# Performance work log

Measured on AMD Instinct MI355X. Metric: run time of the kernel, lower is better.

The kernel has to match this reference:

```python
import jax, jax.numpy as jnp
import numpy as np

MC, IN_C, OUT_C, K, STRIDE, PAD = 10, 16, 32, 3, 2, 1
D = IN_C * K * K  # 144


def setup_inputs() -> dict:
    key = jax.random.key(0)
    k1, k2 = jax.random.split(key)
    x = jax.random.normal(k1, (8, IN_C, 128, 128), dtype=jnp.float32)
    theta_logsigma = jnp.zeros((1,), jnp.float32)
    Omega_mean = jnp.zeros((D, OUT_C), jnp.float32)
    # init: theta_llscale * -2 = -log(in*k*k)
    Omega_logsigma = jnp.full((D, OUT_C), -np.log(float(D)), jnp.float32)
    Omega_eps = jax.random.normal(k2, (MC, D, OUT_C), dtype=jnp.float32)
    return {"x": x, "theta_logsigma": theta_logsigma, "Omega_mean": Omega_mean,
            "Omega_logsigma": Omega_logsigma, "Omega_eps": Omega_eps}


def reference(x, theta_logsigma, Omega_mean, Omega_logsigma, Omega_eps):
    B, _, H, W = x.shape
    # reparameterized weights: [mc, D, out]
    Omega = Omega_eps * jnp.exp(Omega_logsigma * 0.5) + Omega_mean
    # torch: view(mc,k,k,in,out).permute(0,4,3,1,2).reshape(mc*out,in,k,k)
    w = Omega.reshape(MC, K, K, IN_C, OUT_C).transpose(0, 4, 3, 1, 2)
    w = w.reshape(MC * OUT_C, IN_C, K, K)
    # F0 path: replicate x over mc -> [B, mc*in, H, W]
    xr = jnp.broadcast_to(x[None], (MC, B, IN_C, H, W)).transpose(1, 0, 2, 3, 4)
    xr = xr.reshape(B, MC * IN_C, H, W)
    phi_half = jax.lax.conv_general_dilated(
        xr, w, window_strides=(STRIDE, STRIDE),
        padding=[(PAD, PAD), (PAD, PAD)],
        dimension_numbers=("NCHW", "OIHW", "NCHW"),
        feature_group_count=MC)
    hw = phi_half.shape[-1]
    N_rf = OUT_C * hw * hw
    scale = jnp.exp(0.5 * theta_logsigma[0]) / jnp.sqrt(jnp.asarray(N_rf, x.dtype))
    ph = phi_half.reshape(B, MC, OUT_C, hw, hw)
    phi = jnp.concatenate([scale * jnp.cos(ph), scale * jnp.sin(ph)], axis=2)
    return phi.reshape(B, MC * 2 * OUT_C, hw, hw)
```

## Files before the change

kernel.cpp:

```cpp
#include <hip/hip_runtime.h>
#include <hip/hip_bf16.h>
#include <math.h>

#define MC_    10
#define IN_C_  16
#define OUT_C_ 32
#define K_     3
#define D_     (IN_C_ * K_ * K_)
#define H_     128
#define W_     128
#define HW_    64
#define B_     8

__global__ __launch_bounds__(256) void prep_w_kernel(
    const float* __restrict__ eps, const float* __restrict__ logsig,
    const float* __restrict__ mean, float* __restrict__ w)
{
    int i = blockIdx.x * 256 + threadIdx.x;
    if (i < MC_ * D_ * OUT_C_) {
        int doc = i % (D_ * OUT_C_);
        w[i] = eps[i] * __expf(0.5f * logsig[doc]) + mean[doc];
    }
}

__global__ __launch_bounds__(256) void conv_rff_kernel(
    const float* __restrict__ x,
    const float* __restrict__ w,
    const float* __restrict__ theta,
    float* __restrict__ out)
{
    const int tid    = threadIdx.x;
    const int lane   = tid & 63;
    const int waveid = tid >> 6;
    const int oh     = blockIdx.x * 4 + waveid;
    const int mc     = blockIdx.y;
    const int b      = blockIdx.z;
    const int ow     = lane;

    const float scale = __expf(0.5f * theta[0]) *
                        rsqrtf((float)(OUT_C_ * HW_ * HW_));

    float acc[OUT_C_];
#pragma unroll
    for (int oc = 0; oc < OUT_C_; ++oc) acc[oc] = 0.0f;

    const float* __restrict__ wmc = w + (size_t)mc * (D_ * OUT_C_);
    const float* __restrict__ xb  = x + (size_t)b * IN_C_ * H_ * W_;
    const int ih0 = oh * 2 - 1;
    const int iw0 = ow * 2 - 1;

    for (int ic = 0; ic < IN_C_; ++ic) {
        const float* __restrict__ xc = xb + (size_t)ic * (H_ * W_);
        float xv[9];
#pragma unroll
        for (int kh = 0; kh < 3; ++kh) {
#pragma unroll
            for (int kw = 0; kw < 3; ++kw) {
                const int ih = ih0 + kh;
                const int iw = iw0 + kw;
                const bool ok = ((unsigned)ih < (unsigned)H_) &&
                                ((unsigned)iw < (unsigned)W_);
                xv[kh * 3 + kw] = ok ? xc[ih * W_ + iw] : 0.0f;
            }
        }
#pragma unroll
        for (int t = 0; t < 9; ++t) {
            const float* __restrict__ wp = wmc + (size_t)(t * IN_C_ + ic) * OUT_C_;
            const float xt = xv[t];
#pragma unroll
            for (int oc = 0; oc < OUT_C_; ++oc)
                acc[oc] = fmaf(xt, wp[oc], acc[oc]);
        }
    }

    float* __restrict__ op = out +
        (((size_t)b * (MC_ * 2 * OUT_C_) + (size_t)mc * (2 * OUT_C_)) * (HW_ * HW_)) +
        (size_t)oh * HW_ + ow;
#pragma unroll
    for (int oc = 0; oc < OUT_C_; ++oc) {
        float s, c;
        __sincosf(acc[oc], &s, &c);
        op[(size_t)oc * (HW_ * HW_)]              = scale * c;
        op[(size_t)(oc + OUT_C_) * (HW_ * HW_)]   = scale * s;
    }
}

extern "C" void kernel_launch(void* const* d_in, const int* in_sizes, int n_in,
                              void* d_out, int out_size, void* d_ws, size_t ws_size,
                              hipStream_t stream)
{
    const float* x      = (const float*)d_in[0];
    const float* theta  = (const float*)d_in[1];
    const float* mean   = (const float*)d_in[2];
    const float* logsig = (const float*)d_in[3];
    const float* eps    = (const float*)d_in[4];
    float* out = (float*)d_out;
    float* W   = (float*)d_ws;

    const int n_w = MC_ * D_ * OUT_C_;
    prep_w_kernel<<<(n_w + 255) / 256, 256, 0, stream>>>(eps, logsig, mean, W);

    dim3 grid(HW_ / 4, MC_, B_);
    conv_rff_kernel<<<grid, 256, 0, stream>>>(x, W, theta, out);
}
```

Measured before the change: 135.2 us.

## Rewrite grouped conv as bf16 MFMA GEMM with im2col tile shared across MC

Replaces the per-thread FP32 FMA convolution with an im2col tile staged in LDS as bf16 and multiplied with MFMA 16x16x32 instructions. The weights are prepacked in bf16, transposed and padded to K=160. Each block now handles one 32-pixel row segment and loops over all 10 MC samples, so the input patch is reused instead of reloaded per MC. Results go through LDS so that sin/cos outputs are written as coalesced float4 stores. Rounding activations and weights to bf16 lowers precision of the phase argument, which may hurt accuracy after cos/sin.

```diff
diff --git a/kernel.cpp b/kernel.cpp
--- a/kernel.cpp
+++ b/kernel.cpp
@@ -6,82 +6,125 @@
 #define IN_C_  16
 #define OUT_C_ 32
 #define K_     3
-#define D_     (IN_C_ * K_ * K_)
+#define D_     144
+#define KP_    160
 #define H_     128
 #define W_     128
 #define HW_    64
 #define B_     8
 
+typedef __attribute__((ext_vector_type(8))) short short8;
+typedef __attribute__((ext_vector_type(4))) float f32x4;
+
+static __device__ __forceinline__ unsigned short f2bf(float v) {
+    union { float f; unsigned u; } x; x.f = v;
+    unsigned r = x.u + 0x7fff + ((x.u >> 16) & 1);
+    return (unsigned short)(r >> 16);
+}
+
 __global__ __launch_bounds__(256) void prep_w_kernel(
     const float* __restrict__ eps, const float* __restrict__ logsig,
-    const float* __restrict__ mean, float* __restrict__ w)
+    const float* __restrict__ mean, unsigned short* __restrict__ w2)
 {
     int i = blockIdx.x * 256 + threadIdx.x;
-    if (i < MC_ * D_ * OUT_C_) {
-        int doc = i % (D_ * OUT_C_);
-        w[i] = eps[i] * __expf(0.5f * logsig[doc]) + mean[doc];
+    if (i >= MC_ * OUT_C_ * KP_) return;
+    int k  = i % KP_;
+    int oc = (i / KP_) % OUT_C_;
+    int mc = i / (KP_ * OUT_C_);
+    float val = 0.0f;
+    if (k < D_) {
+        int doc = k * OUT_C_ + oc;
+        val = eps[mc * (D_ * OUT_C_) + doc] * __expf(0.5f * logsig[doc]) + mean[doc];
     }
+    w2[i] = f2bf(val);
 }
 
-__global__ __launch_bounds__(256) void conv_rff_kernel(
+__global__ __launch_bounds__(256) void conv_rff_mfma(
     const float* __restrict__ x,
-    const float* __restrict__ w,
+    const unsigned short* __restrict__ w2,
     const float* __restrict__ theta,
     float* __restrict__ out)
 {
-    const int tid    = threadIdx.x;
-    const int lane   = tid & 63;
-    const int waveid = tid >> 6;
-    const int oh     = blockIdx.x * 4 + waveid;
-    const int mc     = blockIdx.y;
-    const int b      = blockIdx.z;
-    const int ow     = lane;
+    __shared__ __align__(16) unsigned short Alds[32 * 168];
+    __shared__ __align__(16) float Clds[32 * 36];
 
-    const float scale = __expf(0.5f * theta[0]) *
-                        rsqrtf((float)(OUT_C_ * HW_ * HW_));
+    const int tid  = threadIdx.x;
+    const int tile = blockIdx.x;
+    const int b    = blockIdx.y;
+    const int oh   = tile >> 1;
+    const int ow0  = (tile & 1) << 5;
+    const float* __restrict__ xb = x + (size_t)b * (IN_C_ * H_ * W_);
 
-    float acc[OUT_C_];
 #pragma unroll
-    for (int oc = 0; oc < OUT_C_; ++oc) acc[oc] = 0.0f;
+    for (int j = 0; j < 20; ++j) {
+        int idx = j * 256 + tid;
+        int m = idx & 31;
+        int k = idx >> 5;
+        float val = 0.0f;
+        if (k < D_) {
+            int ic = k & 15;
+            int t  = k >> 4;
+            int kh = (t * 11) >> 5;
+            int kw = t - kh * 3;
+            int ih = oh * 2 - 1 + kh;
+            int iw = (ow0 + m) * 2 - 1 + kw;
+            if ((unsigned)ih < (unsigned)H_ && (unsigned)iw < (unsigned)W_)
+                val = xb[ic * (H_ * W_) + ih * W_ + iw];
+        }
+        Alds[m * 168 + k] = f2bf(val);
+    }
+    __syncthreads();
 
-    const float* __restrict__ wmc = w + (size_t)mc * (D_ * OUT_C_);
-    const float* __restrict__ xb  = x + (size_t)b * IN_C_ * H_ * W_;
-    const int ih0 = oh * 2 - 1;
-    const int iw0 = ow * 2 - 1;
+    const int lane = tid & 63;
+    const int wave = tid >> 6;
+    const int wm   = (wave >> 1) << 4;
+    const int wn   = (wave & 1) << 4;
+    const int l15  = lane & 15;
+    const int quad = lane >> 4;
 
-    for (int ic = 0; ic < IN_C_; ++ic) {
-        const float* __restrict__ xc = xb + (size_t)ic * (H_ * W_);
-        float xv[9];
+    short8 af[5];
 #pragma unroll
-        for (int kh = 0; kh < 3; ++kh) {
+    for (int ks = 0; ks < 5; ++ks)
+        af[ks] = *(const short8*)&Alds[(wm + l15) * 168 + ks * 32 + quad * 8];
+
+    const float scale = __expf(0.5f * theta[0]) * rsqrtf((float)(OUT_C_ * HW_ * HW_));
+
+    const int  rid    = tid >> 2;
+    const int  q      = tid & 3;
+    const int  ocr    = rid & 31;
+    const bool is_cos = rid < 32;
+
+    float* __restrict__ outb =
+        out + (size_t)b * (MC_ * 2 * OUT_C_ * HW_ * HW_) + oh * HW_ + ow0;
+
+    for (int mc = 0; mc < MC_; ++mc) {
+        const unsigned short* __restrict__ wmc = w2 + (size_t)mc * (OUT_C_ * KP_);
+        short8 bfr[5];
 #pragma unroll
-            for (int kw = 0; kw < 3; ++kw) {
-                const int ih = ih0 + kh;
-                const int iw = iw0 + kw;
-                const bool ok = ((unsigned)ih < (unsigned)H_) &&
-                                ((unsigned)iw < (unsigned)W_);
-                xv[kh * 3 + kw] = ok ? xc[ih * W_ + iw] : 0.0f;
-            }
-        }
+        for (int ks = 0; ks < 5; ++ks)
+            bfr[ks] = *(const short8*)&wmc[(wn + l15) * KP_ + ks * 32 + quad * 8];
+
+        f32x4 acc = {0.f, 0.f, 0.f, 0.f};
 #pragma unroll
-        for (int t = 0; t < 9; ++t) {
-            const float* __restrict__ wp = wmc + (size_t)(t * IN_C_ + ic) * OUT_C_;
-            const float xt = xv[t];
+        for (int ks = 0; ks < 5; ++ks)
+            acc = __builtin_amdgcn_mfma_f32_16x16x32_bf16(af[ks], bfr[ks], acc, 0, 0, 0);
+
+        __syncthreads();
 #pragma unroll
-            for (int oc = 0; oc < OUT_C_; ++oc)
-                acc[oc] = fmaf(xt, wp[oc], acc[oc]);
-        }
-    }
+        for (int r = 0; r < 4; ++r)
+            Clds[(wn + l15) * 36 + wm + quad * 4 + r] = acc[r];
+        __syncthreads();
 
-    float* __restrict__ op = out +
-        (((size_t)b * (MC_ * 2 * OUT_C_) + (size_t)mc * (2 * OUT_C_)) * (HW_ * HW_)) +
-        (size_t)oh * HW_ + ow;
+        float4 p0 = *(const float4*)&Clds[ocr * 36 + q * 8];
+        float4 p1 = *(const float4*)&Clds[ocr * 36 + q * 8 + 4];
+        float v[8];
+        float ph[8] = {p0.x, p0.y, p0.z, p0.w, p1.x, p1.y, p1.z, p1.w};
 #pragma unroll
-    for (int oc = 0; oc < OUT_C_; ++oc) {
-        float s, c;
-        __sincosf(acc[oc], &s, &c);
-        op[(size_t)oc * (HW_ * HW_)]              = scale * c;
-        op[(size_t)(oc + OUT_C_) * (HW_ * HW_)]   = scale * s;
+        for (int i = 0; i < 8; ++i)
+            v[i] = scale * (is_cos ? __cosf(ph[i]) : __sinf(ph[i]));
+        float* __restrict__ po = outb + (size_t)(mc * 64 + rid) * (HW_ * HW_) + q * 8;
+        *(float4*)po       = make_float4(v[0], v[1], v[2], v[3]);
+        *((float4*)po + 1) = make_float4(v[4], v[5], v[6], v[7]);
     }
 }
 
@@ -95,11 +138,11 @@
     const float* logsig = (const float*)d_in[3];
     const float* eps    = (const float*)d_in[4];
     float* out = (float*)d_out;
-    float* W   = (float*)d_ws;
+    unsigned short* W2 = (unsigned short*)d_ws;
 
-    const int n_w = MC_ * D_ * OUT_C_;
-    prep_w_kernel<<<(n_w + 255) / 256, 256, 0, stream>>>(eps, logsig, mean, W);
+    const int n_w = MC_ * OUT_C_ * KP_;
+    prep_w_kernel<<<(n_w + 255) / 256, 256, 0, stream>>>(eps, logsig, mean, W2);
 
-    dim3 grid(HW_ / 4, MC_, B_);
-    conv_rff_kernel<<<grid, 256, 0, stream>>>(x, W, theta, out);
+    dim3 grid(128, B_);
+    conv_rff_mfma<<<grid, 256, 0, stream>>>(x, W2, theta, out);
 }
```

Result: faster. 118.2 us (-12.6%).
